# Kernel optimization log

Measured on AMD Instinct MI355X. Metric: run time of the kernel, lower is better.

Reference implementation:

```python
import jax, jax.numpy as jnp
import numpy as np

D_MODEL = 1024
D_INTERNAL = 64
SEQ = 2048
BATCH = 4


def setup_inputs() -> dict:
    key = jax.random.key(0)
    ks = jax.random.split(key, 9)
    s = 1.0 / np.sqrt(D_MODEL)
    return {
        "query": jax.random.normal(ks[0], (SEQ, BATCH, D_MODEL), jnp.float32),
        "key": jax.random.normal(ks[1], (SEQ, BATCH, D_MODEL), jnp.float32),
        "value": jax.random.normal(ks[2], (SEQ, BATCH, D_MODEL), jnp.float32),
        "Wq": jax.random.normal(ks[3], (D_MODEL, D_INTERNAL), jnp.float32) * s,
        "bq": jnp.zeros((D_INTERNAL,), jnp.float32),
        "Wk": jax.random.normal(ks[4], (D_MODEL, D_INTERNAL), jnp.float32) * s,
        "bk": jnp.zeros((D_INTERNAL,), jnp.float32),
        "Wv": jax.random.normal(ks[5], (D_MODEL, D_MODEL), jnp.float32) * s,
        "bv": jnp.zeros((D_MODEL,), jnp.float32),
    }


def reference(query, key, value, Wq, bq, Wk, bk, Wv, bv):
    # inputs: (S, B, D); project then move batch first -> (B, S, *)
    q = (query @ Wq + bq).transpose(1, 0, 2)          # (B, S, d_int)
    k = (key @ Wk + bk).transpose(1, 0, 2)            # (B, S, d_int)
    v = (value @ Wv + bv).transpose(1, 0, 2)          # (B, S, D)
    scores = jnp.einsum("bqd,bkd->bqk", q, k) / jnp.sqrt(jnp.float32(D_INTERNAL))
    probs = jax.nn.softmax(scores, axis=-1)           # row softmax over keys
    # extra renormalization over the QUERY axis (dim=1), as in the source
    probs = probs / (1e-9 + probs.sum(axis=1, keepdims=True))
    aten = jnp.einsum("bqk,bkd->bqd", probs, v).transpose(1, 0, 2)  # (S, B, D)
    return aten, probs
```

## Files before the change

kernel.cpp:

```cpp
#include <hip/hip_runtime.h>
#include <math.h>

#define SEQ 2048
#define BATCH 4
#define DM 1024
#define DI 64

typedef __attribute__((ext_vector_type(8))) short bf16x8;
typedef __attribute__((ext_vector_type(4))) float f32x4;

__device__ __forceinline__ unsigned short f2bf(float f) {
  unsigned u = __float_as_uint(f);
  unsigned r = (u + 0x7fff + ((u >> 16) & 1)) >> 16;
  return (unsigned short)r;
}

__device__ __forceinline__ float bf2f(unsigned short u) {
  return __uint_as_float((unsigned)u << 16);
}

__device__ __forceinline__ void gload_lds16(const void* g, void* l) {
  __builtin_amdgcn_global_load_lds(
      (const __attribute__((address_space(1))) unsigned int*)g,
      (__attribute__((address_space(3))) unsigned int*)l, 16, 0, 0);
}


__global__ __launch_bounds__(256) void wqkt_kernel(
    const float* __restrict__ Wq, const float* __restrict__ Wk,
    unsigned short* __restrict__ WqkT) {
  __shared__ unsigned short t[64][65];
  const float* W = blockIdx.y ? Wk : Wq;
  unsigned short* WT = WqkT + (size_t)blockIdx.y * DI * DM;
  int bx = blockIdx.x * 64;
  int lx = threadIdx.x & 63, ly = threadIdx.x >> 6;
#pragma unroll
  for (int i = 0; i < 64; i += 4)
    t[ly + i][lx] = f2bf(W[(size_t)(bx + ly + i) * DI + lx]);
  __syncthreads();
#pragma unroll
  for (int i = 0; i < 64; i += 4)
    WT[(size_t)(ly + i) * DM + bx + lx] = t[lx][ly + i];
}

__global__ __launch_bounds__(256) void wvt_kernel(
    const float* __restrict__ W, unsigned short* __restrict__ WT) {
  __shared__ unsigned short t[64][65];
  int bx = blockIdx.x * 64, by = blockIdx.y * 64;
  int lx = threadIdx.x & 63, ly = threadIdx.x >> 6;
#pragma unroll
  for (int i = 0; i < 64; i += 4)
    t[ly + i][lx] = f2bf(W[(size_t)(bx + ly + i) * DM + by + lx]);
  __syncthreads();
#pragma unroll
  for (int i = 0; i < 64; i += 4)
    WT[(size_t)(by + ly + i) * DM + bx + lx] = t[lx][ly + i];
}

__global__ __launch_bounds__(256) void qkproj_mfma(
    const float* __restrict__ query, const float* __restrict__ key,
    const unsigned short* __restrict__ WqkT,
    const float* __restrict__ bq, const float* __restrict__ bk,
    unsigned short* __restrict__ qbf, unsigned short* __restrict__ kbf) {
  __shared__ __align__(16) unsigned short As[32 * 32];
  __shared__ __align__(16) unsigned short Bs[64 * 32];
  int which = blockIdx.y;
  const float* A = (which ? key : query) + (size_t)blockIdx.x * 32 * DM;
  const unsigned short* Bt = WqkT + (size_t)which * DI * DM;
  const float* bias = which ? bk : bq;
  unsigned short* outp = which ? kbf : qbf;

  const int tid = threadIdx.x;
  const int lane = tid & 63, wave = tid >> 6;
  const int lrow = lane & 15, quad = lane >> 4;
  const int wr = (wave >> 1) * 16;
  const int wc = (wave & 1) * 32;
  const int sw = (quad ^ ((lrow >> 1) & 3)) * 8;
  f32x4 acc[2] = {};

  const int am = tid >> 3, asub = tid & 7;
  const int akc = asub * 4;
  const int asl = am * 32 + (((asub >> 1) ^ ((am >> 1) & 3)) * 8) + (asub & 1) * 4;
  const int bn = tid >> 2;
  const int bkc = (((tid & 3) ^ ((bn >> 1) & 3)) * 8);

  for (int k0 = 0; k0 < DM; k0 += 32) {
    __syncthreads();
    gload_lds16(Bt + (size_t)bn * DM + k0 + bkc, Bs + wave * 512);
    float4 a = *(const float4*)(A + (size_t)am * DM + k0 + akc);
    ushort4 h;
    h.x = f2bf(a.x); h.y = f2bf(a.y); h.z = f2bf(a.z); h.w = f2bf(a.w);
    *(ushort4*)&As[asl] = h;
    __syncthreads();
    bf16x8 af = *(const bf16x8*)&As[(wr + lrow) * 32 + sw];
    bf16x8 b0 = *(const bf16x8*)&Bs[(wc + lrow) * 32 + sw];
    bf16x8 b1 = *(const bf16x8*)&Bs[(wc + 16 + lrow) * 32 + sw];
    acc[0] = __builtin_amdgcn_mfma_f32_16x16x32_bf16(af, b0, acc[0], 0, 0, 0);
    acc[1] = __builtin_amdgcn_mfma_f32_16x16x32_bf16(af, b1, acc[1], 0, 0, 0);
  }
  int sbase = blockIdx.x * 8 + (wr >> 2) + quad;
#pragma unroll
  for (int ni = 0; ni < 2; ++ni) {
    int n = wc + ni * 16 + lrow;
    float bb = bias[n];
#pragma unroll
    for (int reg = 0; reg < 4; ++reg)
      outp[((size_t)reg * SEQ + sbase) * DI + n] = f2bf(acc[ni][reg] + bb);
  }
}

__global__ __launch_bounds__(256) void vcast_kernel(
    const float* __restrict__ value, unsigned short* __restrict__ vbf) {
  size_t i = ((size_t)blockIdx.x * 256 + threadIdx.x) * 8;
  float4 a = *(const float4*)(value + i);
  float4 b = *(const float4*)(value + i + 4);
  bf16x8 h;
  h[0] = (short)f2bf(a.x); h[1] = (short)f2bf(a.y);
  h[2] = (short)f2bf(a.z); h[3] = (short)f2bf(a.w);
  h[4] = (short)f2bf(b.x); h[5] = (short)f2bf(b.y);
  h[6] = (short)f2bf(b.z); h[7] = (short)f2bf(b.w);
  *(bf16x8*)(vbf + i) = h;
}

__device__ __forceinline__ void mfma_core_bb(
    const unsigned short* __restrict__ At, int lda,
    const unsigned short* __restrict__ Bt, int ldb,
    int K, f32x4 (&acc)[4][4],
    unsigned short* As, unsigned short* Bs) {
  const int tid  = threadIdx.x;
  const int lane = tid & 63;
  const int wave = tid >> 6;
  const int wr   = (wave >> 1) * 64;
  const int wc   = (wave & 1) * 64;
  const int lrow = lane & 15;
  const int quad = lane >> 4;
  const int sw   = (quad ^ ((lrow >> 1) & 3)) * 8;

  for (int k0 = 0; k0 < K; k0 += 32) {
    __syncthreads();
#pragma unroll
    for (int it = 0; it < 2; ++it) {
      int c = it * 256 + wave * 64 + lane;
      int m = c >> 2, kc = ((c & 3) ^ ((c >> 3) & 3)) * 8;
      gload_lds16(At + (size_t)m * lda + k0 + kc,
                  As + (size_t)(it * 256 + wave * 64) * 8);
    }
#pragma unroll
    for (int it = 0; it < 2; ++it) {
      int c = it * 256 + wave * 64 + lane;
      int n = c >> 2, kc = ((c & 3) ^ ((c >> 3) & 3)) * 8;
      gload_lds16(Bt + (size_t)n * ldb + k0 + kc,
                  Bs + (size_t)(it * 256 + wave * 64) * 8);
    }
    __syncthreads();
    bf16x8 af[4], bfr[4];
#pragma unroll
    for (int mi = 0; mi < 4; ++mi)
      af[mi] = *(const bf16x8*)&As[(wr + mi * 16 + lrow) * 32 + sw];
#pragma unroll
    for (int ni = 0; ni < 4; ++ni)
      bfr[ni] = *(const bf16x8*)&Bs[(wc + ni * 16 + lrow) * 32 + sw];
#pragma unroll
    for (int mi = 0; mi < 4; ++mi)
#pragma unroll
      for (int ni = 0; ni < 4; ++ni)
        acc[mi][ni] = __builtin_amdgcn_mfma_f32_16x16x32_bf16(
            af[mi], bfr[ni], acc[mi][ni], 0, 0, 0);
  }
}

__device__ __forceinline__ void mfma_core_bb_12864(
    const unsigned short* __restrict__ At, int lda,
    const unsigned short* __restrict__ Bt, int ldb,
    int K, f32x4 (&acc)[4][2],
    unsigned short* As, unsigned short* Bs) {
  const int tid  = threadIdx.x;
  const int lane = tid & 63;
  const int wave = tid >> 6;
  const int wr   = (wave >> 1) * 64;
  const int wc   = (wave & 1) * 32;
  const int lrow = lane & 15;
  const int quad = lane >> 4;
  const int sw   = (quad ^ ((lrow >> 1) & 3)) * 8;
  const int bn   = tid >> 2;
  const int bkc  = ((tid & 3) ^ ((bn >> 1) & 3)) * 8;

  for (int k0 = 0; k0 < K; k0 += 32) {
    __syncthreads();
#pragma unroll
    for (int it = 0; it < 2; ++it) {
      int c = it * 256 + tid;
      int m = c >> 2, kc = ((c & 3) ^ ((m >> 1) & 3)) * 8;
      gload_lds16(At + (size_t)m * lda + k0 + kc,
                  As + (size_t)(it * 256 + wave * 64) * 8);
    }
    gload_lds16(Bt + (size_t)bn * ldb + k0 + bkc, Bs + wave * 512);
    __syncthreads();
    bf16x8 af[4], bfr[2];
#pragma unroll
    for (int mi = 0; mi < 4; ++mi)
      af[mi] = *(const bf16x8*)&As[(wr + mi * 16 + lrow) * 32 + sw];
#pragma unroll
    for (int ni = 0; ni < 2; ++ni)
      bfr[ni] = *(const bf16x8*)&Bs[(wc + ni * 16 + lrow) * 32 + sw];
#pragma unroll
    for (int mi = 0; mi < 4; ++mi)
#pragma unroll
      for (int ni = 0; ni < 2; ++ni)
        acc[mi][ni] = __builtin_amdgcn_mfma_f32_16x16x32_bf16(
            af[mi], bfr[ni], acc[mi][ni], 0, 0, 0);
  }
}

__global__ __launch_bounds__(256) void vproj_mfma(
    const unsigned short* __restrict__ vbf, const unsigned short* __restrict__ WvT,
    const float* __restrict__ bv, unsigned short* __restrict__ vT) {
  __shared__ __align__(16) unsigned short As[128 * 32];
  __shared__ __align__(16) unsigned short Bs[64 * 32];
  __shared__ __align__(16) unsigned short ep[64 * 4 * 32];
  f32x4 acc[4][2] = {};
  int m0 = blockIdx.x * 128, n0 = blockIdx.y * 64;
  mfma_core_bb_12864(vbf + (size_t)m0 * DM, DM, WvT + (size_t)n0 * DM, DM, DM,
                     acc, As, Bs);
  const int tid = threadIdx.x;
  const int lane = tid & 63, wave = tid >> 6;
  const int wr = (wave >> 1) * 64, wc = (wave & 1) * 32;
  const int lrow = lane & 15, quad = lane >> 4;
#pragma unroll
  for (int mi = 0; mi < 4; ++mi) {
    int ss = (wr >> 2) + mi * 4 + quad;
#pragma unroll
    for (int ni = 0; ni < 2; ++ni) {
      int nn = wc + ni * 16 + lrow;
      float bias = bv[n0 + nn];
      int swz = (nn & 3) << 3;
#pragma unroll
      for (int reg = 0; reg < 4; ++reg)
        ep[nn * 128 + reg * 32 + (ss ^ swz)] = f2bf(acc[mi][ni][reg] + bias);
    }
  }
  __syncthreads();
  int s0 = m0 >> 2;
#pragma unroll
  for (int t8 = 0; t8 < 4; ++t8) {
    int c = t8 * 256 + tid;
    int ss8 = (c & 3) * 8, b = (c >> 2) & 3, nn = c >> 4;
    uint4 vv = *(const uint4*)&ep[nn * 128 + b * 32 + (ss8 ^ ((nn & 3) << 3))];
    *(uint4*)&vT[((size_t)(b * DM + n0 + nn)) * SEQ + s0 + ss8] = vv;
  }
}

__global__ __launch_bounds__(256) void scores_mfma(
    const unsigned short* __restrict__ qbf, const unsigned short* __restrict__ kbf,
    unsigned short* __restrict__ ebf, float* __restrict__ rowsum) {
  __shared__ __align__(16) unsigned short As[128 * 32];
  __shared__ __align__(16) unsigned short Bs[128 * 32];
  int b = blockIdx.z;
  f32x4 acc[4][4] = {};
  mfma_core_bb(qbf + ((size_t)b * SEQ + blockIdx.x * 128) * DI, DI,
               kbf + ((size_t)b * SEQ + blockIdx.y * 128) * DI, DI, DI,
               acc, As, Bs);
  unsigned short* C = ebf + (size_t)b * SEQ * SEQ;
  float* rs = rowsum + (size_t)b * SEQ;
  const int lane = threadIdx.x & 63, wave = threadIdx.x >> 6;
  const int wr = (wave >> 1) * 64, wc = (wave & 1) * 64;
  const int lrow = lane & 15, quad = lane >> 4;
#pragma unroll
  for (int mi = 0; mi < 4; ++mi) {
    int qr = blockIdx.x * 128 + wr + mi * 16 + quad * 4;
    float r0 = 0.f, r1 = 0.f, r2 = 0.f, r3 = 0.f;
#pragma unroll
    for (int ni = 0; ni < 4; ++ni) {
      int n = blockIdx.y * 128 + wc + ni * 16 + lrow;
      float e0 = __expf(acc[mi][ni][0] * 0.125f);
      float e1 = __expf(acc[mi][ni][1] * 0.125f);
      float e2 = __expf(acc[mi][ni][2] * 0.125f);
      float e3 = __expf(acc[mi][ni][3] * 0.125f);
      C[(size_t)(qr + 0) * SEQ + n] = f2bf(e0);
      C[(size_t)(qr + 1) * SEQ + n] = f2bf(e1);
      C[(size_t)(qr + 2) * SEQ + n] = f2bf(e2);
      C[(size_t)(qr + 3) * SEQ + n] = f2bf(e3);
      r0 += e0; r1 += e1; r2 += e2; r3 += e3;
    }
    r0 += __shfl_xor(r0, 1); r0 += __shfl_xor(r0, 2);
    r0 += __shfl_xor(r0, 4); r0 += __shfl_xor(r0, 8);
    r1 += __shfl_xor(r1, 1); r1 += __shfl_xor(r1, 2);
    r1 += __shfl_xor(r1, 4); r1 += __shfl_xor(r1, 8);
    r2 += __shfl_xor(r2, 1); r2 += __shfl_xor(r2, 2);
    r2 += __shfl_xor(r2, 4); r2 += __shfl_xor(r2, 8);
    r3 += __shfl_xor(r3, 1); r3 += __shfl_xor(r3, 2);
    r3 += __shfl_xor(r3, 4); r3 += __shfl_xor(r3, 8);
    if (lrow == 0) {
      atomicAdd(&rs[qr + 0], r0);
      atomicAdd(&rs[qr + 1], r1);
      atomicAdd(&rs[qr + 2], r2);
      atomicAdd(&rs[qr + 3], r3);
    }
  }
}

__global__ void zero_kernel(float* __restrict__ p, int n) {
  int i = blockIdx.x * blockDim.x + threadIdx.x;
  if (i < n) p[i] = 0.f;
}

__global__ void recip_kernel(const float* __restrict__ in,
                             float* __restrict__ outp, float eps, int n) {
  int i = blockIdx.x * blockDim.x + threadIdx.x;
  if (i < n) outp[i] = 1.0f / (eps + in[i]);
}

__global__ __launch_bounds__(256) void colsum_kernel(
    const unsigned short* __restrict__ ebf, const float* __restrict__ invrs,
    float* __restrict__ colsum) {
  int b = blockIdx.z;
  int k = blockIdx.x * 256 + threadIdx.x;
  int q0 = blockIdx.y * 128;
  const unsigned short* p = ebf + (size_t)b * SEQ * SEQ + (size_t)q0 * SEQ + k;
  const float* ir = invrs + (size_t)b * SEQ + q0;
  float sum = 0.f;
#pragma unroll 4
  for (int i = 0; i < 128; ++i) sum += bf2f(p[(size_t)i * SEQ]) * ir[i];
  atomicAdd(&colsum[b * SEQ + k], sum);
}

__global__ __launch_bounds__(256) void vscale_kernel(
    unsigned short* __restrict__ vT, const float* __restrict__ invcol) {
  size_t i = ((size_t)blockIdx.x * 256 + threadIdx.x) * 8;
  int s = (int)(i & (SEQ - 1));
  int b = (int)(i >> 21);
  bf16x8 v = *(const bf16x8*)(vT + i);
  const float* ic = invcol + (size_t)b * SEQ + s;
  float4 c0 = *(const float4*)(ic);
  float4 c1 = *(const float4*)(ic + 4);
  bf16x8 r;
  r[0] = (short)f2bf(bf2f((unsigned short)v[0]) * c0.x);
  r[1] = (short)f2bf(bf2f((unsigned short)v[1]) * c0.y);
  r[2] = (short)f2bf(bf2f((unsigned short)v[2]) * c0.z);
  r[3] = (short)f2bf(bf2f((unsigned short)v[3]) * c0.w);
  r[4] = (short)f2bf(bf2f((unsigned short)v[4]) * c1.x);
  r[5] = (short)f2bf(bf2f((unsigned short)v[5]) * c1.y);
  r[6] = (short)f2bf(bf2f((unsigned short)v[6]) * c1.z);
  r[7] = (short)f2bf(bf2f((unsigned short)v[7]) * c1.w);
  *(bf16x8*)(vT + i) = r;
}

__global__ __launch_bounds__(256) void probsout_kernel(
    const unsigned short* __restrict__ ebf, const float* __restrict__ invrs,
    const float* __restrict__ invcol, float* __restrict__ probs) {
  size_t f = ((size_t)blockIdx.x * 256 + threadIdx.x) * 4;
  int b = (int)(f >> 22);
  int q = (int)((f >> 11) & 2047);
  int k = (int)(f & 2047);
  ushort4 h = *(const ushort4*)(ebf + f);
  float ir = invrs[b * SEQ + q];
  float4 c = *(const float4*)(invcol + b * SEQ + k);
  float4 p;
  p.x = bf2f(h.x) * ir * c.x;
  p.y = bf2f(h.y) * ir * c.y;
  p.z = bf2f(h.z) * ir * c.z;
  p.w = bf2f(h.w) * ir * c.w;
  *(float4*)(probs + f) = p;
}

__global__ __launch_bounds__(256) void aten_mfma(
    const unsigned short* __restrict__ ebf, const unsigned short* __restrict__ vT,
    const float* __restrict__ invrs, float* __restrict__ out) {
  __shared__ __align__(16) unsigned short As[128 * 32];
  __shared__ __align__(16) unsigned short Bs[128 * 32];
  __shared__ float irs[128];
  int bid = blockIdx.x;
  int wg = (bid & 7) * 64 + (bid >> 3);
  int mb = wg & 15, nb = (wg >> 4) & 7, b = wg >> 7;
  int m0 = mb * 128, n0 = nb * 128;
  if (threadIdx.x < 128)
    irs[threadIdx.x] = invrs[(size_t)b * SEQ + m0 + threadIdx.x];
  f32x4 acc[4][4] = {};
  mfma_core_bb(ebf + ((size_t)b * SEQ + m0) * SEQ, SEQ,
               vT + ((size_t)b * DM + n0) * SEQ, SEQ, SEQ, acc, As, Bs);
  const int lane = threadIdx.x & 63, wave = threadIdx.x >> 6;
  const int wr = (wave >> 1) * 64, wc = (wave & 1) * 64;
  const int lrow = lane & 15, quad = lane >> 4;
#pragma unroll
  for (int mi = 0; mi < 4; ++mi) {
    int rb = wr + mi * 16 + quad * 4;
    int qr = m0 + rb;
#pragma unroll
    for (int ni = 0; ni < 4; ++ni) {
      int n = n0 + wc + ni * 16 + lrow;
#pragma unroll
      for (int reg = 0; reg < 4; ++reg)
        out[(size_t)(qr + reg) * (BATCH * DM) + b * DM + n] =
            acc[mi][ni][reg] * irs[rb + reg];
    }
  }
}

extern "C" void kernel_launch(void* const* d_in, const int* in_sizes, int n_in,
                              void* d_out, int out_size, void* d_ws, size_t ws_size,
                              hipStream_t stream) {
  const float* query = (const float*)d_in[0];
  const float* key   = (const float*)d_in[1];
  const float* value = (const float*)d_in[2];
  const float* Wq    = (const float*)d_in[3];
  const float* bq    = (const float*)d_in[4];
  const float* Wk    = (const float*)d_in[5];
  const float* bk    = (const float*)d_in[6];
  const float* Wv    = (const float*)d_in[7];
  const float* bv    = (const float*)d_in[8];

  float* out   = (float*)d_out;
  float* probs = out + (size_t)SEQ * BATCH * DM;

  unsigned short* WvT  = (unsigned short*)d_ws;
  unsigned short* WqkT = WvT  + (size_t)DM * DM;
  unsigned short* qbf  = WqkT + (size_t)2 * DI * DM;
  unsigned short* kbf  = qbf  + (size_t)BATCH * SEQ * DI;
  unsigned short* vT   = kbf  + (size_t)BATCH * SEQ * DI;
  unsigned short* ebf  = vT   + (size_t)BATCH * DM * SEQ;
  unsigned short* vbf  = ebf;
  float* rowsum = (float*)(ebf + (size_t)BATCH * SEQ * SEQ);
  float* colsum = rowsum + (size_t)BATCH * SEQ;
  float* invrs  = colsum + (size_t)BATCH * SEQ;
  float* invcol = invrs  + (size_t)BATCH * SEQ;

  wqkt_kernel<<<dim3(16, 2), 256, 0, stream>>>(Wq, Wk, WqkT);
  qkproj_mfma<<<dim3(SEQ * BATCH / 32, 2), 256, 0, stream>>>(
      query, key, WqkT, bq, bk, qbf, kbf);
  wvt_kernel<<<dim3(16, 16), 256, 0, stream>>>(Wv, WvT);
  vcast_kernel<<<(SEQ * BATCH * DM / 8) / 256, 256, 0, stream>>>(value, vbf);
  vproj_mfma<<<dim3(SEQ * BATCH / 128, DM / 64), 256, 0, stream>>>(vbf, WvT, bv, vT);
  zero_kernel<<<(2 * BATCH * SEQ + 255) / 256, 256, 0, stream>>>(rowsum, 2 * BATCH * SEQ);
  scores_mfma<<<dim3(SEQ / 128, SEQ / 128, BATCH), 256, 0, stream>>>(
      qbf, kbf, ebf, rowsum);
  recip_kernel<<<(BATCH * SEQ + 255) / 256, 256, 0, stream>>>(
      rowsum, invrs, 0.0f, BATCH * SEQ);
  colsum_kernel<<<dim3(SEQ / 256, SEQ / 128, BATCH), 256, 0, stream>>>(
      ebf, invrs, colsum);
  recip_kernel<<<(BATCH * SEQ + 255) / 256, 256, 0, stream>>>(
      colsum, invcol, 1e-9f, BATCH * SEQ);
  vscale_kernel<<<(BATCH * DM * SEQ / 8) / 256, 256, 0, stream>>>(vT, invcol);
  aten_mfma<<<dim3(512), 256, 0, stream>>>(ebf, vT, invrs, out);
  probsout_kernel<<<(BATCH * SEQ * SEQ / 4) / 256, 256, 0, stream>>>(
      ebf, invrs, invcol, probs);
}
```

Baseline: 330.2 us.

## Row-panel scores kernel with in-block rowsum, merge transposes, deepen aten K tile

Replaces the tiled scores kernel with a row-panel kernel where each block covers 16 query rows across all keys. It reduces row sums in-block and writes the reciprocals directly, which removes the atomics, the rowsum zeroing and one recip launch. The two weight-transpose kernels are merged into one launch. The aten GEMM now uses a K tile of 64 instead of 32, halving barrier count per K step. The row-panel scores kernel stores bf16 scalars with a 16-row panel and little reuse, which may lower MFMA efficiency.

Measured after the change: 327.3 us. About the same (-0.9%).

```diff
diff --git a/kernel.cpp b/kernel.cpp
--- a/kernel.cpp
+++ b/kernel.cpp
@@ -26,35 +26,34 @@
 }
 
 
-__global__ __launch_bounds__(256) void wqkt_kernel(
+__global__ __launch_bounds__(256) void trans_kernel(
     const float* __restrict__ Wq, const float* __restrict__ Wk,
-    unsigned short* __restrict__ WqkT) {
+    const float* __restrict__ Wv,
+    unsigned short* __restrict__ WqkT, unsigned short* __restrict__ WvT) {
   __shared__ unsigned short t[64][65];
-  const float* W = blockIdx.y ? Wk : Wq;
-  unsigned short* WT = WqkT + (size_t)blockIdx.y * DI * DM;
-  int bx = blockIdx.x * 64;
   int lx = threadIdx.x & 63, ly = threadIdx.x >> 6;
-#pragma unroll
-  for (int i = 0; i < 64; i += 4)
-    t[ly + i][lx] = f2bf(W[(size_t)(bx + ly + i) * DI + lx]);
-  __syncthreads();
-#pragma unroll
-  for (int i = 0; i < 64; i += 4)
-    WT[(size_t)(ly + i) * DM + bx + lx] = t[lx][ly + i];
-}
-
-__global__ __launch_bounds__(256) void wvt_kernel(
-    const float* __restrict__ W, unsigned short* __restrict__ WT) {
-  __shared__ unsigned short t[64][65];
-  int bx = blockIdx.x * 64, by = blockIdx.y * 64;
-  int lx = threadIdx.x & 63, ly = threadIdx.x >> 6;
-#pragma unroll
-  for (int i = 0; i < 64; i += 4)
-    t[ly + i][lx] = f2bf(W[(size_t)(bx + ly + i) * DM + by + lx]);
-  __syncthreads();
-#pragma unroll
-  for (int i = 0; i < 64; i += 4)
-    WT[(size_t)(by + ly + i) * DM + bx + lx] = t[lx][ly + i];
+  if (blockIdx.y < 16) {
+    int bx = blockIdx.x * 64, by = blockIdx.y * 64;
+#pragma unroll
+    for (int i = 0; i < 64; i += 4)
+      t[ly + i][lx] = f2bf(Wv[(size_t)(bx + ly + i) * DM + by + lx]);
+    __syncthreads();
+#pragma unroll
+    for (int i = 0; i < 64; i += 4)
+      WvT[(size_t)(by + ly + i) * DM + bx + lx] = t[lx][ly + i];
+  } else {
+    int which = blockIdx.y - 16;
+    const float* W = which ? Wk : Wq;
+    unsigned short* WT = WqkT + (size_t)which * DI * DM;
+    int bx = blockIdx.x * 64;
+#pragma unroll
+    for (int i = 0; i < 64; i += 4)
+      t[ly + i][lx] = f2bf(W[(size_t)(bx + ly + i) * DI + lx]);
+    __syncthreads();
+#pragma unroll
+    for (int i = 0; i < 64; i += 4)
+      WT[(size_t)(ly + i) * DM + bx + lx] = t[lx][ly + i];
+  }
 }
 
 __global__ __launch_bounds__(256) void qkproj_mfma(
@@ -120,53 +119,6 @@
   h[4] = (short)f2bf(b.x); h[5] = (short)f2bf(b.y);
   h[6] = (short)f2bf(b.z); h[7] = (short)f2bf(b.w);
   *(bf16x8*)(vbf + i) = h;
-}
-
-__device__ __forceinline__ void mfma_core_bb(
-    const unsigned short* __restrict__ At, int lda,
-    const unsigned short* __restrict__ Bt, int ldb,
-    int K, f32x4 (&acc)[4][4],
-    unsigned short* As, unsigned short* Bs) {
-  const int tid  = threadIdx.x;
-  const int lane = tid & 63;
-  const int wave = tid >> 6;
-  const int wr   = (wave >> 1) * 64;
-  const int wc   = (wave & 1) * 64;
-  const int lrow = lane & 15;
-  const int quad = lane >> 4;
-  const int sw   = (quad ^ ((lrow >> 1) & 3)) * 8;
-
-  for (int k0 = 0; k0 < K; k0 += 32) {
-    __syncthreads();
-#pragma unroll
-    for (int it = 0; it < 2; ++it) {
-      int c = it * 256 + wave * 64 + lane;
-      int m = c >> 2, kc = ((c & 3) ^ ((c >> 3) & 3)) * 8;
-      gload_lds16(At + (size_t)m * lda + k0 + kc,
-                  As + (size_t)(it * 256 + wave * 64) * 8);
-    }
-#pragma unroll
-    for (int it = 0; it < 2; ++it) {
-      int c = it * 256 + wave * 64 + lane;
-      int n = c >> 2, kc = ((c & 3) ^ ((c >> 3) & 3)) * 8;
-      gload_lds16(Bt + (size_t)n * ldb + k0 + kc,
-                  Bs + (size_t)(it * 256 + wave * 64) * 8);
-    }
-    __syncthreads();
-    bf16x8 af[4], bfr[4];
-#pragma unroll
-    for (int mi = 0; mi < 4; ++mi)
-      af[mi] = *(const bf16x8*)&As[(wr + mi * 16 + lrow) * 32 + sw];
-#pragma unroll
-    for (int ni = 0; ni < 4; ++ni)
-      bfr[ni] = *(const bf16x8*)&Bs[(wc + ni * 16 + lrow) * 32 + sw];
-#pragma unroll
-    for (int mi = 0; mi < 4; ++mi)
-#pragma unroll
-      for (int ni = 0; ni < 4; ++ni)
-        acc[mi][ni] = __builtin_amdgcn_mfma_f32_16x16x32_bf16(
-            af[mi], bfr[ni], acc[mi][ni], 0, 0, 0);
-  }
 }
 
 __device__ __forceinline__ void mfma_core_bb_12864(
@@ -250,52 +202,84 @@
   }
 }
 
-__global__ __launch_bounds__(256) void scores_mfma(
+__global__ __launch_bounds__(256) void scores_rowpanel(
     const unsigned short* __restrict__ qbf, const unsigned short* __restrict__ kbf,
-    unsigned short* __restrict__ ebf, float* __restrict__ rowsum) {
-  __shared__ __align__(16) unsigned short As[128 * 32];
-  __shared__ __align__(16) unsigned short Bs[128 * 32];
-  int b = blockIdx.z;
-  f32x4 acc[4][4] = {};
-  mfma_core_bb(qbf + ((size_t)b * SEQ + blockIdx.x * 128) * DI, DI,
-               kbf + ((size_t)b * SEQ + blockIdx.y * 128) * DI, DI, DI,
-               acc, As, Bs);
+    unsigned short* __restrict__ ebf, float* __restrict__ invrs) {
+  __shared__ __align__(16) unsigned short Qs[16 * 64];
+  __shared__ __align__(16) unsigned short Ks[128 * 64];
+  __shared__ float red[4][16];
+  int bid = blockIdx.x;
+  int x = bid & 7, j = bid >> 3;
+  int b = x >> 1;
+  int q0 = (j * 2 + (x & 1)) * 16;
+
+  const int tid = threadIdx.x;
+  const int lane = tid & 63, wave = tid >> 6;
+  const int lrow = lane & 15, quad = lane >> 4;
+  const int wc = wave * 32;
+  const int sw = (quad ^ ((lrow >> 1) & 3)) * 8;
+  const unsigned short* Q = qbf + ((size_t)b * SEQ + q0) * DI;
+  const unsigned short* Kp = kbf + (size_t)b * SEQ * DI;
   unsigned short* C = ebf + (size_t)b * SEQ * SEQ;
-  float* rs = rowsum + (size_t)b * SEQ;
-  const int lane = threadIdx.x & 63, wave = threadIdx.x >> 6;
-  const int wr = (wave >> 1) * 64, wc = (wave & 1) * 64;
-  const int lrow = lane & 15, quad = lane >> 4;
-#pragma unroll
-  for (int mi = 0; mi < 4; ++mi) {
-    int qr = blockIdx.x * 128 + wr + mi * 16 + quad * 4;
-    float r0 = 0.f, r1 = 0.f, r2 = 0.f, r3 = 0.f;
-#pragma unroll
-    for (int ni = 0; ni < 4; ++ni) {
-      int n = blockIdx.y * 128 + wc + ni * 16 + lrow;
-      float e0 = __expf(acc[mi][ni][0] * 0.125f);
-      float e1 = __expf(acc[mi][ni][1] * 0.125f);
-      float e2 = __expf(acc[mi][ni][2] * 0.125f);
-      float e3 = __expf(acc[mi][ni][3] * 0.125f);
-      C[(size_t)(qr + 0) * SEQ + n] = f2bf(e0);
-      C[(size_t)(qr + 1) * SEQ + n] = f2bf(e1);
-      C[(size_t)(qr + 2) * SEQ + n] = f2bf(e2);
-      C[(size_t)(qr + 3) * SEQ + n] = f2bf(e3);
-      r0 += e0; r1 += e1; r2 += e2; r3 += e3;
-    }
-    r0 += __shfl_xor(r0, 1); r0 += __shfl_xor(r0, 2);
-    r0 += __shfl_xor(r0, 4); r0 += __shfl_xor(r0, 8);
-    r1 += __shfl_xor(r1, 1); r1 += __shfl_xor(r1, 2);
-    r1 += __shfl_xor(r1, 4); r1 += __shfl_xor(r1, 8);
-    r2 += __shfl_xor(r2, 1); r2 += __shfl_xor(r2, 2);
-    r2 += __shfl_xor(r2, 4); r2 += __shfl_xor(r2, 8);
-    r3 += __shfl_xor(r3, 1); r3 += __shfl_xor(r3, 2);
-    r3 += __shfl_xor(r3, 4); r3 += __shfl_xor(r3, 8);
-    if (lrow == 0) {
-      atomicAdd(&rs[qr + 0], r0);
-      atomicAdd(&rs[qr + 1], r1);
-      atomicAdd(&rs[qr + 2], r2);
-      atomicAdd(&rs[qr + 3], r3);
-    }
+
+  if (tid < 128) {
+    int m = tid >> 3, kk = (tid >> 2) & 1, jj = tid & 3;
+    gload_lds16(Q + (size_t)m * DI + kk * 32 + ((jj ^ ((m >> 1) & 3)) * 8),
+                Qs + (size_t)(tid & ~63) * 8);
+  }
+
+  float rsum[4] = {0.f, 0.f, 0.f, 0.f};
+  for (int kt = 0; kt < 16; ++kt) {
+    int k0 = kt * 128;
+    __syncthreads();
+#pragma unroll
+    for (int it = 0; it < 4; ++it) {
+      int c = it * 256 + tid;
+      int n = c >> 3, kk = (c >> 2) & 1, jj = c & 3;
+      gload_lds16(Kp + (size_t)(k0 + n) * DI + kk * 32 + ((jj ^ ((n >> 1) & 3)) * 8),
+                  Ks + (size_t)(it * 256 + wave * 64) * 8);
+    }
+    __syncthreads();
+    bf16x8 af[2], bfr[2][2];
+#pragma unroll
+    for (int kk = 0; kk < 2; ++kk) {
+      af[kk] = *(const bf16x8*)&Qs[lrow * 64 + kk * 32 + sw];
+#pragma unroll
+      for (int ni = 0; ni < 2; ++ni)
+        bfr[ni][kk] = *(const bf16x8*)&Ks[(wc + ni * 16 + lrow) * 64 + kk * 32 + sw];
+    }
+    f32x4 acc[2] = {};
+#pragma unroll
+    for (int ni = 0; ni < 2; ++ni) {
+      acc[ni] = __builtin_amdgcn_mfma_f32_16x16x32_bf16(af[0], bfr[ni][0], acc[ni], 0, 0, 0);
+      acc[ni] = __builtin_amdgcn_mfma_f32_16x16x32_bf16(af[1], bfr[ni][1], acc[ni], 0, 0, 0);
+    }
+#pragma unroll
+    for (int ni = 0; ni < 2; ++ni) {
+      int n = k0 + wc + ni * 16 + lrow;
+#pragma unroll
+      for (int reg = 0; reg < 4; ++reg) {
+        float e = __expf(acc[ni][reg] * 0.125f);
+        C[(size_t)(q0 + quad * 4 + reg) * SEQ + n] = f2bf(e);
+        rsum[reg] += e;
+      }
+    }
+  }
+#pragma unroll
+  for (int reg = 0; reg < 4; ++reg) {
+    rsum[reg] += __shfl_xor(rsum[reg], 1);
+    rsum[reg] += __shfl_xor(rsum[reg], 2);
+    rsum[reg] += __shfl_xor(rsum[reg], 4);
+    rsum[reg] += __shfl_xor(rsum[reg], 8);
+  }
+  if (lrow == 0) {
+#pragma unroll
+    for (int reg = 0; reg < 4; ++reg) red[wave][quad * 4 + reg] = rsum[reg];
+  }
+  __syncthreads();
+  if (tid < 16) {
+    float t = red[0][tid] + red[1][tid] + red[2][tid] + red[3][tid];
+    invrs[(size_t)b * SEQ + q0 + tid] = 1.0f / t;
   }
 }
 
@@ -366,8 +350,8 @@
 __global__ __launch_bounds__(256) void aten_mfma(
     const unsigned short* __restrict__ ebf, const unsigned short* __restrict__ vT,
     const float* __restrict__ invrs, float* __restrict__ out) {
-  __shared__ __align__(16) unsigned short As[128 * 32];
-  __shared__ __align__(16) unsigned short Bs[128 * 32];
+  __shared__ __align__(16) unsigned short As[128 * 64];
+  __shared__ __align__(16) unsigned short Bs[128 * 64];
   __shared__ float irs[128];
   int bid = blockIdx.x;
   int wg = (bid & 7) * 64 + (bid >> 3);
@@ -375,12 +359,50 @@
   int m0 = mb * 128, n0 = nb * 128;
   if (threadIdx.x < 128)
     irs[threadIdx.x] = invrs[(size_t)b * SEQ + m0 + threadIdx.x];
-  f32x4 acc[4][4] = {};
-  mfma_core_bb(ebf + ((size_t)b * SEQ + m0) * SEQ, SEQ,
-               vT + ((size_t)b * DM + n0) * SEQ, SEQ, SEQ, acc, As, Bs);
-  const int lane = threadIdx.x & 63, wave = threadIdx.x >> 6;
+  const unsigned short* At = ebf + ((size_t)b * SEQ + m0) * SEQ;
+  const unsigned short* Bt = vT + ((size_t)b * DM + n0) * SEQ;
+
+  const int tid = threadIdx.x;
+  const int lane = tid & 63, wave = tid >> 6;
   const int wr = (wave >> 1) * 64, wc = (wave & 1) * 64;
   const int lrow = lane & 15, quad = lane >> 4;
+  const int sw = (quad ^ ((lrow >> 1) & 3)) * 8;
+
+  f32x4 acc[4][4] = {};
+  for (int k0 = 0; k0 < SEQ; k0 += 64) {
+    __syncthreads();
+#pragma unroll
+    for (int it = 0; it < 4; ++it) {
+      int c = it * 256 + tid;
+      int m = c >> 3, kk = (c >> 2) & 1, jj = c & 3;
+      gload_lds16(At + (size_t)m * SEQ + k0 + kk * 32 + ((jj ^ ((m >> 1) & 3)) * 8),
+                  As + (size_t)(it * 256 + wave * 64) * 8);
+    }
+#pragma unroll
+    for (int it = 0; it < 4; ++it) {
+      int c = it * 256 + tid;
+      int n = c >> 3, kk = (c >> 2) & 1, jj = c & 3;
+      gload_lds16(Bt + (size_t)n * SEQ + k0 + kk * 32 + ((jj ^ ((n >> 1) & 3)) * 8),
+                  Bs + (size_t)(it * 256 + wave * 64) * 8);
+    }
+    __syncthreads();
+    bf16x8 bfr[4][2];
+#pragma unroll
+    for (int ni = 0; ni < 4; ++ni)
+#pragma unroll
+      for (int kk = 0; kk < 2; ++kk)
+        bfr[ni][kk] = *(const bf16x8*)&Bs[(wc + ni * 16 + lrow) * 64 + kk * 32 + sw];
+#pragma unroll
+    for (int mi = 0; mi < 4; ++mi) {
+      bf16x8 a0 = *(const bf16x8*)&As[(wr + mi * 16 + lrow) * 64 + sw];
+      bf16x8 a1 = *(const bf16x8*)&As[(wr + mi * 16 + lrow) * 64 + 32 + sw];
+#pragma unroll
+      for (int ni = 0; ni < 4; ++ni) {
+        acc[mi][ni] = __builtin_amdgcn_mfma_f32_16x16x32_bf16(a0, bfr[ni][0], acc[mi][ni], 0, 0, 0);
+        acc[mi][ni] = __builtin_amdgcn_mfma_f32_16x16x32_bf16(a1, bfr[ni][1], acc[mi][ni], 0, 0, 0);
+      }
+    }
+  }
 #pragma unroll
   for (int mi = 0; mi < 4; ++mi) {
     int rb = wr + mi * 16 + quad * 4;
@@ -419,22 +441,17 @@
   unsigned short* vT   = kbf  + (size_t)BATCH * SEQ * DI;
   unsigned short* ebf  = vT   + (size_t)BATCH * DM * SEQ;
   unsigned short* vbf  = ebf;
-  float* rowsum = (float*)(ebf + (size_t)BATCH * SEQ * SEQ);
-  float* colsum = rowsum + (size_t)BATCH * SEQ;
+  float* colsum = (float*)(ebf + (size_t)BATCH * SEQ * SEQ);
   float* invrs  = colsum + (size_t)BATCH * SEQ;
   float* invcol = invrs  + (size_t)BATCH * SEQ;
 
-  wqkt_kernel<<<dim3(16, 2), 256, 0, stream>>>(Wq, Wk, WqkT);
+  trans_kernel<<<dim3(16, 18), 256, 0, stream>>>(Wq, Wk, Wv, WqkT, WvT);
   qkproj_mfma<<<dim3(SEQ * BATCH / 32, 2), 256, 0, stream>>>(
       query, key, WqkT, bq, bk, qbf, kbf);
-  wvt_kernel<<<dim3(16, 16), 256, 0, stream>>>(Wv, WvT);
   vcast_kernel<<<(SEQ * BATCH * DM / 8) / 256, 256, 0, stream>>>(value, vbf);
   vproj_mfma<<<dim3(SEQ * BATCH / 128, DM / 64), 256, 0, stream>>>(vbf, WvT, bv, vT);
-  zero_kernel<<<(2 * BATCH * SEQ + 255) / 256, 256, 0, stream>>>(rowsum, 2 * BATCH * SEQ);
-  scores_mfma<<<dim3(SEQ / 128, SEQ / 128, BATCH), 256, 0, stream>>>(
-      qbf, kbf, ebf, rowsum);
-  recip_kernel<<<(BATCH * SEQ + 255) / 256, 256, 0, stream>>>(
-      rowsum, invrs, 0.0f, BATCH * SEQ);
+  scores_rowpanel<<<dim3(512), 256, 0, stream>>>(qbf, kbf, ebf, invrs);
+  zero_kernel<<<(BATCH * SEQ + 255) / 256, 256, 0, stream>>>(colsum, BATCH * SEQ);
   colsum_kernel<<<dim3(SEQ / 256, SEQ / 128, BATCH), 256, 0, stream>>>(
       ebf, invrs, colsum);
   recip_kernel<<<(BATCH * SEQ + 255) / 256, 256, 0, stream>>>(
```
